# Kernel optimization log

Hardware: AMD Instinct MI355X
Metric: run time of the kernel (lower is better)

The kernel has to match this reference:

```python
import jax, jax.numpy as jnp
import numpy as np

B, C, H, W_SP, OC, K = 16, 64, 128, 128, 128, 3
SPARSITY = 0.9


def setup_inputs() -> dict:
    key = jax.random.key(0)
    kx, kmask, ksign = jax.random.split(key, 3)
    x = jax.random.normal(kx, (B, C, H, W_SP), dtype=jnp.float32)
    n = OC * C * K * K
    signs = jax.random.bernoulli(ksign, 0.5, (n,)).astype(jnp.float32) * 2.0 - 1.0
    mask = jax.random.bernoulli(kmask, SPARSITY, (n,)).astype(jnp.float32)
    # Original: weight.view((OC, C*K*K)).t() -> (CK, OC) layout used against im2col columns.
    weight = (signs * mask).reshape(OC, C * K * K).T  # (CK, OC)
    return {"x": x, "weight": weight}


def reference(x, weight):
    # Intended math of RandomBinaryConvV1: cols = unfold(x) (B, CK, L);
    # out[b, l, oc] = sum_k cols[b, k, l] * weight[k, oc]  (ternary weight),
    # i.e. a standard 2D convolution with a ternary kernel, 'same' padding, stride 1.
    b, c, h, w = x.shape
    ck, oc = weight.shape
    k = int(round(np.sqrt(ck // c)))  # static shapes -> Python int
    kern = weight.T.reshape(oc, c, k, k)  # OIHW
    pad = k // 2
    out = jax.lax.conv_general_dilated(
        x, kern,
        window_strides=(1, 1),
        padding=[(pad, pad), (pad, pad)],
        dimension_numbers=("NCHW", "OIHW", "NCHW"),
    )
    return out  # (B, OC, H, W)
```

## Files before the change

### kernel.cpp

```cpp
#include <hip/hip_runtime.h>
#include <hip/hip_bf16.h>
#include <cstdint>

#define Cc 64
#define Hh 128
#define Ww 128
#define OCn 128
#define HBLK 4
#define WT 64
#define WLs 72
#define HP 130
#define WP 136
#define NT 18
#define SLOT_SHORTS (WLs * Cc)
#define XP_BYTES (((size_t)16 * HP * WP * Cc) * 2)

typedef float f32x4 __attribute__((ext_vector_type(4)));
typedef __bf16 bf16x8 __attribute__((ext_vector_type(8)));
typedef short s16x8 __attribute__((ext_vector_type(8)));

union bs8 { s16x8 s; bf16x8 b; };
__device__ __forceinline__ bf16x8 as_bf16x8(s16x8 s) { bs8 u; u.s = s; return u.b; }

__global__ __launch_bounds__(256) void prepass_kernel(const float* __restrict__ x,
                                                      unsigned short* __restrict__ xp) {
  int bid = blockIdx.x;
  int hp = bid % HP;
  int b = bid / HP;
  int t = threadIdx.x;
  size_t obase = ((size_t)b * HP + hp) * WP * Cc;
  s16x8 z = (s16x8){0, 0, 0, 0, 0, 0, 0, 0};
  if (hp == 0 || hp == HP - 1) {
    for (int ck = t; ck < WP * Cc / 8; ck += 256)
      *(s16x8*)(xp + obase + (size_t)ck * 8) = z;
    return;
  }
  int h = hp - 1;
  __shared__ float tile[Cc][Ww + 1];
  int w = t & 127, chalf = t >> 7;
#pragma unroll
  for (int k = 0; k < 32; ++k) {
    int c = chalf * 32 + k;
    tile[c][w] = x[(((size_t)b * Cc + c) * Hh + h) * Ww + w];
  }
  __syncthreads();
#pragma unroll
  for (int k = 0; k < 4; ++k) {
    int idx = k * 256 + t;
    int ww = idx >> 3, cg = idx & 7;
    bf16x8 v;
#pragma unroll
    for (int j = 0; j < 8; ++j) v[j] = (__bf16)tile[cg * 8 + j][ww];
    bs8 u; u.b = v;
    *(s16x8*)(xp + obase + (size_t)(ww + 1) * Cc + cg * 8) = u.s;
  }
  if (t < 16) {
    int wz = (t >> 3) ? (Ww + 1) : 0;
    *(s16x8*)(xp + obase + (size_t)wz * Cc + (t & 7) * 8) = z;
  }
}

__global__ void pack_w_kernel(const float* __restrict__ w, s16x8* __restrict__ wp) {
  int idx = blockIdx.x * 256 + threadIdx.x;
  if (idx >= NT * 8 * 64) return;
  int l = idx & 63;
  int mb = (idx >> 6) & 7;
  int t = idx >> 9;
  int ch = t & 1;
  int o = t >> 1;
  int kh = o / 3, kw = o % 3;
  int oc = mb * 16 + (l & 15);
  int kl0 = (l >> 4) * 8;
  bf16x8 v;
#pragma unroll
  for (int j = 0; j < 8; ++j) {
    int c = ch * 32 + kl0 + j;
    int ko = (c * 3 + kh) * 3 + kw;
    v[j] = (__bf16)w[ko * OCn + oc];
  }
  bs8 u; u.b = v;
  wp[idx] = u.s;
}

__global__ __launch_bounds__(256) void conv_mfma_kernel(
    const unsigned short* __restrict__ xp, const s16x8* __restrict__ wpf,
    float* __restrict__ out) {
  __shared__ __align__(16) short xt[4 * SLOT_SHORTS];
  int tid = threadIdx.x;
  int bid = blockIdx.x;
  int wt = bid & 1;
  int hb = (bid >> 1) & 31;
  int b = bid >> 6;
  int h0 = hb * HBLK;
  int wv = tid >> 6, lane = tid & 63;
  int l15 = lane & 15, l4 = lane >> 4;

  auto stage = [&](int h_img) {
    int slot = (h_img + 1) & 3;
    size_t rbase = (((size_t)b * HP + (h_img + 1)) * WP + wt * WT) * Cc;
    int cg = lane & 7, wo = lane >> 3;
    const unsigned short* src0 = xp + rbase + (size_t)wo * Cc + ((cg ^ wo) << 3);
    for (int i = wv; i < 9; i += 4) {
      const unsigned short* src = src0 + (size_t)i * 8 * Cc;
      short* dst = &xt[slot * SLOT_SHORTS + i * 512];
      __builtin_amdgcn_global_load_lds(
          (const __attribute__((address_space(1))) void*)src,
          (__attribute__((address_space(3))) void*)dst, 16, 0, 0);
    }
  };

  stage(h0 - 1);
  stage(h0);
  stage(h0 + 1);

  for (int i = 0; i < HBLK; ++i) {
    int h = h0 + i;
    __syncthreads();
    if (i < HBLK - 1) stage(h + 2);

    f32x4 acc[2][4];
#pragma unroll
    for (int mi = 0; mi < 2; ++mi)
#pragma unroll
      for (int ni = 0; ni < 4; ++ni)
        acc[mi][ni] = (f32x4){0.f, 0.f, 0.f, 0.f};

#pragma unroll
    for (int t = 0; t < NT; ++t) {
      int kh = t / 6, kw = (t >> 1) % 3, ch = t & 1;
      bf16x8 a0 = as_bf16x8(wpf[(t * 8 + wv * 2 + 0) * 64 + lane]);
      bf16x8 a1 = as_bf16x8(wpf[(t * 8 + wv * 2 + 1) * 64 + lane]);
      int slot = (h + kh) & 3;
      int cgr = ch * 4 + l4;
#pragma unroll
      for (int ni = 0; ni < 4; ++ni) {
        int wl2 = ni * 16 + l15 + kw;
        int caddr = slot * SLOT_SHORTS + wl2 * Cc + ((cgr ^ (wl2 & 7)) << 3);
        bf16x8 bfr = as_bf16x8(*(const s16x8*)&xt[caddr]);
        acc[0][ni] = __builtin_amdgcn_mfma_f32_16x16x32_bf16(a0, bfr, acc[0][ni], 0, 0, 0);
        acc[1][ni] = __builtin_amdgcn_mfma_f32_16x16x32_bf16(a1, bfr, acc[1][ni], 0, 0, 0);
      }
    }

#pragma unroll
    for (int mi = 0; mi < 2; ++mi)
#pragma unroll
      for (int ni = 0; ni < 4; ++ni) {
        int oc = wv * 32 + mi * 16 + l4 * 4;
        int w_img = wt * WT + ni * 16 + l15;
        float* po = out + (((size_t)(b * OCn + oc)) * Hh + h) * Ww + w_img;
#pragma unroll
        for (int r = 0; r < 4; ++r)
          __builtin_nontemporal_store(acc[mi][ni][r], po + (size_t)r * Hh * Ww);
      }
  }
}

extern "C" void kernel_launch(void* const* d_in, const int* in_sizes, int n_in,
                              void* d_out, int out_size, void* d_ws, size_t ws_size,
                              hipStream_t stream) {
  const float* x = (const float*)d_in[0];
  const float* w = (const float*)d_in[1];
  float* out = (float*)d_out;
  unsigned short* xp = (unsigned short*)d_ws;
  s16x8* wpf = (s16x8*)((char*)d_ws + XP_BYTES);
  prepass_kernel<<<16 * HP, 256, 0, stream>>>(x, xp);
  pack_w_kernel<<<36, 256, 0, stream>>>(w, wpf);
  conv_mfma_kernel<<<1024, 256, 0, stream>>>(xp, wpf, out);
}
```

Baseline: 63.15 us.

## Fuse NCHW-to-NHWC bf16 conversion into conv kernel staging, drop prepass

Removes the separate prepass kernel that transposed and padded x into a bf16 NHWC workspace. The conv kernel now loads fp32 rows of x directly into registers, zero-fills the borders, converts to bf16 and scatters them into swizzled LDS, with the next row's loads issued before the MFMA loop and the writes done after it. This saves one kernel launch and a full extra read and write of the input through global memory. In exchange it drops the async global_load_lds path, reads each halo row redundantly across blocks, and adds scalar 2-byte LDS stores plus extra registers.

```diff
diff --git a/kernel.cpp b/kernel.cpp
--- a/kernel.cpp
+++ b/kernel.cpp
@@ -9,11 +9,8 @@
 #define HBLK 4
 #define WT 64
 #define WLs 72
-#define HP 130
-#define WP 136
 #define NT 18
 #define SLOT_SHORTS (WLs * Cc)
-#define XP_BYTES (((size_t)16 * HP * WP * Cc) * 2)
 
 typedef float f32x4 __attribute__((ext_vector_type(4)));
 typedef __bf16 bf16x8 __attribute__((ext_vector_type(8)));
@@ -21,44 +18,6 @@
 
 union bs8 { s16x8 s; bf16x8 b; };
 __device__ __forceinline__ bf16x8 as_bf16x8(s16x8 s) { bs8 u; u.s = s; return u.b; }
-
-__global__ __launch_bounds__(256) void prepass_kernel(const float* __restrict__ x,
-                                                      unsigned short* __restrict__ xp) {
-  int bid = blockIdx.x;
-  int hp = bid % HP;
-  int b = bid / HP;
-  int t = threadIdx.x;
-  size_t obase = ((size_t)b * HP + hp) * WP * Cc;
-  s16x8 z = (s16x8){0, 0, 0, 0, 0, 0, 0, 0};
-  if (hp == 0 || hp == HP - 1) {
-    for (int ck = t; ck < WP * Cc / 8; ck += 256)
-      *(s16x8*)(xp + obase + (size_t)ck * 8) = z;
-    return;
-  }
-  int h = hp - 1;
-  __shared__ float tile[Cc][Ww + 1];
-  int w = t & 127, chalf = t >> 7;
-#pragma unroll
-  for (int k = 0; k < 32; ++k) {
-    int c = chalf * 32 + k;
-    tile[c][w] = x[(((size_t)b * Cc + c) * Hh + h) * Ww + w];
-  }
-  __syncthreads();
-#pragma unroll
-  for (int k = 0; k < 4; ++k) {
-    int idx = k * 256 + t;
-    int ww = idx >> 3, cg = idx & 7;
-    bf16x8 v;
-#pragma unroll
-    for (int j = 0; j < 8; ++j) v[j] = (__bf16)tile[cg * 8 + j][ww];
-    bs8 u; u.b = v;
-    *(s16x8*)(xp + obase + (size_t)(ww + 1) * Cc + cg * 8) = u.s;
-  }
-  if (t < 16) {
-    int wz = (t >> 3) ? (Ww + 1) : 0;
-    *(s16x8*)(xp + obase + (size_t)wz * Cc + (t & 7) * 8) = z;
-  }
-}
 
 __global__ void pack_w_kernel(const float* __restrict__ w, s16x8* __restrict__ wp) {
   int idx = blockIdx.x * 256 + threadIdx.x;
@@ -83,7 +42,7 @@
 }
 
 __global__ __launch_bounds__(256) void conv_mfma_kernel(
-    const unsigned short* __restrict__ xp, const s16x8* __restrict__ wpf,
+    const float* __restrict__ x, const s16x8* __restrict__ wpf,
     float* __restrict__ out) {
   __shared__ __align__(16) short xt[4 * SLOT_SHORTS];
   int tid = threadIdx.x;
@@ -94,29 +53,51 @@
   int h0 = hb * HBLK;
   int wv = tid >> 6, lane = tid & 63;
   int l15 = lane & 15, l4 = lane >> 4;
+  int ws = wt * WT - 4;
 
-  auto stage = [&](int h_img) {
+  auto stage_load = [&](int h_img, f32x4* r) {
+    bool hok = (h_img >= 0) && (h_img < Hh);
+    const float* base = x + (((size_t)(b * Cc + lane)) * Hh + (hok ? h_img : 0)) * Ww;
+#pragma unroll
+    for (int p = 0; p < 5; ++p) {
+      int g = wv + 4 * p;
+      int p0 = ws + g * 4;
+      bool ok = hok && (g < 18) && (p0 >= 0) && (p0 < Ww);
+      r[p] = ok ? *(const f32x4*)(base + p0) : (f32x4){0.f, 0.f, 0.f, 0.f};
+    }
+  };
+  auto stage_write = [&](int h_img, const f32x4* r) {
     int slot = (h_img + 1) & 3;
-    size_t rbase = (((size_t)b * HP + (h_img + 1)) * WP + wt * WT) * Cc;
-    int cg = lane & 7, wo = lane >> 3;
-    const unsigned short* src0 = xp + rbase + (size_t)wo * Cc + ((cg ^ wo) << 3);
-    for (int i = wv; i < 9; i += 4) {
-      const unsigned short* src = src0 + (size_t)i * 8 * Cc;
-      short* dst = &xt[slot * SLOT_SHORTS + i * 512];
-      __builtin_amdgcn_global_load_lds(
-          (const __attribute__((address_space(1))) void*)src,
-          (__attribute__((address_space(3))) void*)dst, 16, 0, 0);
+    short* sb = &xt[slot * SLOT_SHORTS];
+#pragma unroll
+    for (int p = 0; p < 5; ++p) {
+      int g = wv + 4 * p;
+      if (g >= 18) continue;
+#pragma unroll
+      for (int j = 0; j < 4; ++j) {
+        int wl = g * 4 + j - 3;
+        if (wl < 0 || wl >= 66) continue;
+        __bf16 v = (__bf16)r[p][j];
+        sb[wl * Cc + (lane ^ ((wl & 7) << 3))] = *(short*)&v;
+      }
     }
   };
 
-  stage(h0 - 1);
-  stage(h0);
-  stage(h0 + 1);
+  {
+    f32x4 r0[5], r1[5], r2[5];
+    stage_load(h0 - 1, r0);
+    stage_load(h0, r1);
+    stage_load(h0 + 1, r2);
+    stage_write(h0 - 1, r0);
+    stage_write(h0, r1);
+    stage_write(h0 + 1, r2);
+  }
 
+  f32x4 pre[5];
   for (int i = 0; i < HBLK; ++i) {
     int h = h0 + i;
     __syncthreads();
-    if (i < HBLK - 1) stage(h + 2);
+    if (i < HBLK - 1) stage_load(h + 2, pre);
 
     f32x4 acc[2][4];
 #pragma unroll
@@ -153,6 +134,8 @@
         for (int r = 0; r < 4; ++r)
           __builtin_nontemporal_store(acc[mi][ni][r], po + (size_t)r * Hh * Ww);
       }
+
+    if (i < HBLK - 1) stage_write(h + 2, pre);
   }
 }
 
@@ -162,9 +145,7 @@
   const float* x = (const float*)d_in[0];
   const float* w = (const float*)d_in[1];
   float* out = (float*)d_out;
-  unsigned short* xp = (unsigned short*)d_ws;
-  s16x8* wpf = (s16x8*)((char*)d_ws + XP_BYTES);
-  prepass_kernel<<<16 * HP, 256, 0, stream>>>(x, xp);
+  s16x8* wpf = (s16x8*)d_ws;
   pack_w_kernel<<<36, 256, 0, stream>>>(w, wpf);
-  conv_mfma_kernel<<<1024, 256, 0, stream>>>(xp, wpf, out);
+  conv_mfma_kernel<<<1024, 256, 0, stream>>>(x, (const s16x8*)wpf, out);
 }
```

Measured after the change: 97.65 us. 1.55x slower.

## Merge weight packing into prepass and swizzle block order for XCD locality

Applied to the files above, without the earlier changes.

Folds the weight-packing kernel into the input prepass launch as extra blocks, removing one kernel launch and its gap. Remaps block indices in both the prepass and the conv kernel so that consecutive blocks are spread across the 8 XCDs in contiguous chunks, aiming to improve L2 locality for the halo rows each conv block shares with its neighbours. Uses nontemporal loads for the fp32 input, which is read only once. The remapping assumes the grid sizes are multiples of 8.

```diff
diff --git a/kernel.cpp b/kernel.cpp
--- a/kernel.cpp
+++ b/kernel.cpp
@@ -14,6 +14,7 @@
 #define NT 18
 #define SLOT_SHORTS (WLs * Cc)
 #define XP_BYTES (((size_t)16 * HP * WP * Cc) * 2)
+#define PRE_BLOCKS (16 * HP)
 
 typedef float f32x4 __attribute__((ext_vector_type(4)));
 typedef __bf16 bf16x8 __attribute__((ext_vector_type(8)));
@@ -23,11 +24,34 @@
 __device__ __forceinline__ bf16x8 as_bf16x8(s16x8 s) { bs8 u; u.s = s; return u.b; }
 
 __global__ __launch_bounds__(256) void prepass_kernel(const float* __restrict__ x,
-                                                      unsigned short* __restrict__ xp) {
+                                                      const float* __restrict__ w,
+                                                      unsigned short* __restrict__ xp,
+                                                      s16x8* __restrict__ wpf) {
   int bid = blockIdx.x;
-  int hp = bid % HP;
-  int b = bid / HP;
   int t = threadIdx.x;
+  if (bid >= PRE_BLOCKS) {
+    int idx = (bid - PRE_BLOCKS) * 256 + t;
+    int l = idx & 63;
+    int mb = (idx >> 6) & 7;
+    int tt = idx >> 9;
+    int ch = tt & 1;
+    int o = tt >> 1;
+    int kh = o / 3, kw = o % 3;
+    int oc = mb * 16 + (l & 15);
+    int kl0 = (l >> 4) * 8;
+    bf16x8 v;
+#pragma unroll
+    for (int j = 0; j < 8; ++j) {
+      int c = ch * 32 + kl0 + j;
+      int ko = (c * 3 + kh) * 3 + kw;
+      v[j] = (__bf16)w[ko * OCn + oc];
+    }
+    bs8 u; u.b = v;
+    wpf[idx] = u.s;
+    return;
+  }
+  int u = (bid >> 3) + (bid & 7) * 260;
+  int b = u / 130, hp = u - b * 130;
   size_t obase = ((size_t)b * HP + hp) * WP * Cc;
   s16x8 z = (s16x8){0, 0, 0, 0, 0, 0, 0, 0};
   if (hp == 0 || hp == HP - 1) {
@@ -37,11 +61,12 @@
   }
   int h = hp - 1;
   __shared__ float tile[Cc][Ww + 1];
-  int w = t & 127, chalf = t >> 7;
+  int wpx = t & 127, chalf = t >> 7;
 #pragma unroll
   for (int k = 0; k < 32; ++k) {
     int c = chalf * 32 + k;
-    tile[c][w] = x[(((size_t)b * Cc + c) * Hh + h) * Ww + w];
+    tile[c][wpx] = __builtin_nontemporal_load(
+        &x[(((size_t)b * Cc + c) * Hh + h) * Ww + wpx]);
   }
   __syncthreads();
 #pragma unroll
@@ -51,35 +76,13 @@
     bf16x8 v;
 #pragma unroll
     for (int j = 0; j < 8; ++j) v[j] = (__bf16)tile[cg * 8 + j][ww];
-    bs8 u; u.b = v;
-    *(s16x8*)(xp + obase + (size_t)(ww + 1) * Cc + cg * 8) = u.s;
+    bs8 uu; uu.b = v;
+    *(s16x8*)(xp + obase + (size_t)(ww + 1) * Cc + cg * 8) = uu.s;
   }
   if (t < 16) {
     int wz = (t >> 3) ? (Ww + 1) : 0;
     *(s16x8*)(xp + obase + (size_t)wz * Cc + (t & 7) * 8) = z;
   }
-}
-
-__global__ void pack_w_kernel(const float* __restrict__ w, s16x8* __restrict__ wp) {
-  int idx = blockIdx.x * 256 + threadIdx.x;
-  if (idx >= NT * 8 * 64) return;
-  int l = idx & 63;
-  int mb = (idx >> 6) & 7;
-  int t = idx >> 9;
-  int ch = t & 1;
-  int o = t >> 1;
-  int kh = o / 3, kw = o % 3;
-  int oc = mb * 16 + (l & 15);
-  int kl0 = (l >> 4) * 8;
-  bf16x8 v;
-#pragma unroll
-  for (int j = 0; j < 8; ++j) {
-    int c = ch * 32 + kl0 + j;
-    int ko = (c * 3 + kh) * 3 + kw;
-    v[j] = (__bf16)w[ko * OCn + oc];
-  }
-  bs8 u; u.b = v;
-  wp[idx] = u.s;
 }
 
 __global__ __launch_bounds__(256) void conv_mfma_kernel(
@@ -88,9 +91,10 @@
   __shared__ __align__(16) short xt[4 * SLOT_SHORTS];
   int tid = threadIdx.x;
   int bid = blockIdx.x;
-  int wt = bid & 1;
-  int hb = (bid >> 1) & 31;
-  int b = bid >> 6;
+  int wk = (bid >> 3) + (bid & 7) * 128;
+  int wt = wk & 1;
+  int hb = (wk >> 1) & 31;
+  int b = wk >> 6;
   int h0 = hb * HBLK;
   int wv = tid >> 6, lane = tid & 63;
   int l15 = lane & 15, l4 = lane >> 4;
@@ -164,7 +168,6 @@
   float* out = (float*)d_out;
   unsigned short* xp = (unsigned short*)d_ws;
   s16x8* wpf = (s16x8*)((char*)d_ws + XP_BYTES);
-  prepass_kernel<<<16 * HP, 256, 0, stream>>>(x, xp);
-  pack_w_kernel<<<36, 256, 0, stream>>>(w, wpf);
-  conv_mfma_kernel<<<1024, 256, 0, stream>>>(xp, wpf, out);
+  prepass_kernel<<<PRE_BLOCKS + 36, 256, 0, stream>>>(x, w, xp, wpf);
+  conv_mfma_kernel<<<1024, 256, 0, stream>>>(xp, (const s16x8*)wpf, out);
 }
```

New measurement: 62.28 us. About the same (-1.4%).
